# Kernel tuning notes

Measured on AMD Instinct MI355X. Metric: run time of the kernel, lower is better.

Reference implementation:

```python
import jax, jax.numpy as jnp
import numpy as np

IN_SIZE = 784
Z_DIM = 128
K_DIM = 8192
BATCH = 16384
ENC_HIDDEN = [512, 256]          # EncoderMLP default
DEC_SIZES = [Z_DIM, 256, 512, 784]  # DecoderMLP default: [latent, *hidden]


def _linear(x, w, b):
    return x @ w + b


def find_nearest(query, target):
    # Faithful to: sqrt(sum((Q-T)^2, -1)).min(1)[1]; sqrt is monotone so
    # argmin of squared distance is identical. Computed via the GEMM
    # expansion instead of materializing the (N,K,D) broadcast tensor.
    q2 = jnp.sum(query * query, axis=1, keepdims=True)        # [N,1]
    t2 = jnp.sum(target * target, axis=1)                     # [K]
    d2 = q2 - 2.0 * (query @ target.T) + t2[None, :]          # [N,K]
    idx = jnp.argmin(d2, axis=1)
    return target[idx]


def setup_inputs() -> dict:
    key = jax.random.key(0)
    ks = jax.random.split(key, 16)
    s = 0.02
    inp = {"X": jax.random.uniform(ks[0], (BATCH, 1, 28, 28), dtype=jnp.float32)}
    # Encoder: 784 -> 512 -> 256 (mlp blocks, ReLU) -> 128 (plain Linear)
    enc_sizes = [IN_SIZE] + ENC_HIDDEN + [Z_DIM]
    for i, (din, dout) in enumerate(zip(enc_sizes, enc_sizes[1:]), 1):
        inp[f"enc_w{i}"] = s * jax.random.normal(ks[i], (din, dout), dtype=jnp.float32)
        inp[f"enc_b{i}"] = jnp.zeros((dout,), dtype=jnp.float32)
    # Codebook
    inp["codebook"] = jax.random.normal(ks[8], (K_DIM, Z_DIM), dtype=jnp.float32)
    # Decoder: 128 -> 256 -> 512 -> 784 (mlp blocks, ReLU) + sigmoid out
    for i, (din, dout) in enumerate(zip(DEC_SIZES, DEC_SIZES[1:]), 1):
        inp[f"dec_w{i}"] = s * jax.random.normal(ks[8 + i], (din, dout), dtype=jnp.float32)
        inp[f"dec_b{i}"] = jnp.zeros((dout,), dtype=jnp.float32)
    return inp


def reference(X, enc_w1, enc_b1, enc_w2, enc_b2, enc_w3, enc_b3, codebook,
              dec_w1, dec_b1, dec_w2, dec_b2, dec_w3, dec_b3):
    x = X.reshape(-1, IN_SIZE)
    # Encoder (mlp_block = Linear+ReLU, final layer plain Linear)
    h = jax.nn.relu(_linear(x, enc_w1, enc_b1))
    h = jax.nn.relu(_linear(h, enc_w2, enc_b2))
    z_enc = _linear(h, enc_w3, enc_b3)                         # [N, Z]
    # Nearest codebook vector for each encoding
    z_dec = find_nearest(z_enc, codebook)                      # [N, Z]
    # Decoder
    d = jax.nn.relu(_linear(z_dec, dec_w1, dec_b1))
    d = jax.nn.relu(_linear(d, dec_w2, dec_b2))
    d = jax.nn.relu(_linear(d, dec_w3, dec_b3))
    x_recon = jax.nn.sigmoid(d).reshape(-1, 1, 28, 28)
    # Nearest encoding for each codebook vector (for embedding loss)
    z_enc_for_embd = find_nearest(codebook, z_enc)             # [K, Z]
    return (x_recon, z_enc, z_dec, z_enc_for_embd)
```

## Files before the change

kernel.cpp:

```cpp
#include <hip/hip_runtime.h>
#include <math.h>

using u16 = unsigned short;
using u32 = unsigned int;
using u64 = unsigned long long;

typedef __bf16 bf16x8 __attribute__((ext_vector_type(8)));
typedef short  s16x8  __attribute__((ext_vector_type(8)));
typedef float  f32x4  __attribute__((ext_vector_type(4)));

__device__ __forceinline__ float b2f(u16 u){
  union { u32 i; float f; } x; x.i = ((u32)u) << 16; return x.f;
}
__device__ __forceinline__ u16 f2b(float f){
  union { float f; u32 i; } x; x.f = f;
  u32 i = x.i;
  u32 r = (i + 0x7fffu + ((i >> 16) & 1u)) >> 16;
  return (u16)r;
}
__device__ __forceinline__ f32x4 mfma16(s16x8 a, s16x8 b, f32x4 c){
  return __builtin_amdgcn_mfma_f32_16x16x32_bf16(
      __builtin_bit_cast(bf16x8, a), __builtin_bit_cast(bf16x8, b), c, 0, 0, 0);
}
__device__ __forceinline__ u64 shfl_xor_u64(u64 v, int m){
  int lo = __shfl_xor((int)(u32)v, m);
  int hi = __shfl_xor((int)(u32)(v >> 32), m);
  return ((u64)(u32)hi << 32) | (u32)lo;
}
__device__ __forceinline__ u64 umin64(u64 a, u64 b){ return a < b ? a : b; }
__device__ __forceinline__ u64 packmin(float v, int idx){
  u32 b = __float_as_uint(v);
  b = (b & 0x80000000u) ? ~b : (b | 0x80000000u);
  return ((u64)b << 32) | (u32)idx;
}

__global__ __launch_bounds__(256) void canary_k(float* out, float code){
  out[threadIdx.x] = code;
}

__global__ __launch_bounds__(256) void prep_weights(
    const float* __restrict__ w1, const float* __restrict__ w2, const float* __restrict__ w3,
    const float* __restrict__ dw1, const float* __restrict__ dw2, const float* __restrict__ dw3,
    const float* __restrict__ cb,
    u16* __restrict__ o1h, u16* __restrict__ o1l, u16* __restrict__ o2h, u16* __restrict__ o2l,
    u16* __restrict__ o3h, u16* __restrict__ o3l, u16* __restrict__ o4h, u16* __restrict__ o4l,
    u16* __restrict__ o5h, u16* __restrict__ o5l, u16* __restrict__ o6h, u16* __restrict__ o6l,
    u16* __restrict__ cbh, u16* __restrict__ cbl)
{
  size_t o = (size_t)blockIdx.x * 256 + threadIdx.x;
  if (o >= 1155072){
    size_t e = o - 1155072;
    if (e >= 1048576) return;
    float v = cb[e];
    u16 h = f2b(v);
    cbh[e] = h;
    cbl[e] = f2b(v - b2f(h));
    return;
  }
  const float* src; u16 *hi, *lo; int K, N, Kp; size_t base;
  if      (o <  425984){ src=w1;  hi=o1h; lo=o1l; K=784; N=512; Kp=832; base=0; }
  else if (o <  557056){ src=w2;  hi=o2h; lo=o2l; K=512; N=256; Kp=512; base=425984; }
  else if (o <  589824){ src=w3;  hi=o3h; lo=o3l; K=256; N=128; Kp=256; base=557056; }
  else if (o <  622592){ src=dw1; hi=o4h; lo=o4l; K=128; N=256; Kp=128; base=589824; }
  else if (o <  753664){ src=dw2; hi=o5h; lo=o5l; K=256; N=512; Kp=256; base=622592; }
  else                 { src=dw3; hi=o6h; lo=o6l; K=512; N=784; Kp=512; base=753664; }
  size_t e = o - base;
  int n = (int)(e / Kp), kp = (int)(e % Kp);
  u16 h = 0, l = 0;
  if (kp < K){
    float v = src[(size_t)kp * N + n];
    h = f2b(v);
    l = f2b(v - b2f(h));
  }
  hi[e] = h; lo[e] = l;
}

__global__ __launch_bounds__(256) void norms_all(const float* __restrict__ z, const float* __restrict__ cb,
                                                 float* __restrict__ q2, float* __restrict__ t2){
  int i = blockIdx.x * 256 + threadIdx.x;
  const float* src; float* dst;
  if (i < 16384){ src = z + (size_t)i * 128; dst = q2 + i; }
  else { int j = i - 16384; src = cb + (size_t)j * 128; dst = t2 + j; }
  const float4* r = (const float4*)src;
  float s = 0.f;
  for (int k = 0; k < 32; k++){
    float4 p = r[k];
    s += p.x * p.x + p.y * p.y + p.z * p.z + p.w * p.w;
  }
  *dst = s;
}

template<int ACT, int OUTP>
__global__ __launch_bounds__(256, 2) void gemm_af32(
    const float* __restrict__ A, const u16* __restrict__ B0, const u16* __restrict__ B1,
    const float* __restrict__ bias, float* __restrict__ Cf,
    u16* __restrict__ P0, u16* __restrict__ P1,
    int Astr, int KLIM, int Kp, int KT, int N, int nRowsB)
{
  __shared__ __align__(16) u16 Ah[128][72];
  __shared__ __align__(16) u16 Al[128][72];
  __shared__ __align__(16) u16 Bh[128][72];
  __shared__ __align__(16) u16 Bl[128][72];
  const int tid = threadIdx.x;
  const int m0 = blockIdx.y * 128, n0 = blockIdx.x * 128;
  const int wave = tid >> 6, lane = tid & 63;
  const int wm = (wave >> 1) * 64, wn = (wave & 1) * 64;
  const int quad = lane >> 4, l15 = lane & 15;
  f32x4 acc[4][4] = {};

  for (int kt = 0; kt < KT; ++kt){
    const int kb = kt * 64;
    #pragma unroll
    for (int c = 0; c < 8; c++){
      int idx = c * 256 + tid;
      int r = idx >> 4, c4 = (idx & 15) * 4;
      float4 v = make_float4(0.f, 0.f, 0.f, 0.f);
      if (kb + c4 < KLIM)
        v = *(const float4*)(A + (size_t)(m0 + r) * Astr + kb + c4);
      ushort4 h, l;
      h.x = f2b(v.x); l.x = f2b(v.x - b2f(h.x));
      h.y = f2b(v.y); l.y = f2b(v.y - b2f(h.y));
      h.z = f2b(v.z); l.z = f2b(v.z - b2f(h.z));
      h.w = f2b(v.w); l.w = f2b(v.w - b2f(h.w));
      *(ushort4*)&Ah[r][c4] = h;
      *(ushort4*)&Al[r][c4] = l;
    }
    #pragma unroll
    for (int c = 0; c < 4; c++){
      int idx = c * 256 + tid;
      int r = idx >> 3, col = (idx & 7) * 8;
      int rb = n0 + r; rb = rb < nRowsB ? rb : nRowsB - 1;
      *(uint4*)&Bh[r][col] = *(const uint4*)(B0 + (size_t)rb * Kp + kb + col);
      *(uint4*)&Bl[r][col] = *(const uint4*)(B1 + (size_t)rb * Kp + kb + col);
    }
    __syncthreads();
    #pragma unroll
    for (int kh = 0; kh < 2; ++kh){
      s16x8 ah[4], al[4], bh[4], bl[4];
      #pragma unroll
      for (int t4 = 0; t4 < 4; t4++){
        ah[t4] = *(const s16x8*)&Ah[wm + t4 * 16 + l15][kh * 32 + quad * 8];
        al[t4] = *(const s16x8*)&Al[wm + t4 * 16 + l15][kh * 32 + quad * 8];
        bh[t4] = *(const s16x8*)&Bh[wn + t4 * 16 + l15][kh * 32 + quad * 8];
        bl[t4] = *(const s16x8*)&Bl[wn + t4 * 16 + l15][kh * 32 + quad * 8];
      }
      #pragma unroll
      for (int mt = 0; mt < 4; mt++)
        #pragma unroll
        for (int nt = 0; nt < 4; nt++){
          acc[mt][nt] = mfma16(ah[mt], bh[nt], acc[mt][nt]);
          acc[mt][nt] = mfma16(ah[mt], bl[nt], acc[mt][nt]);
          acc[mt][nt] = mfma16(al[mt], bh[nt], acc[mt][nt]);
        }
    }
    __syncthreads();
  }

  float bvs[4]; int cols[4];
  #pragma unroll
  for (int nt = 0; nt < 4; nt++){
    int cN = n0 + wn + nt * 16 + l15;
    cols[nt] = cN;
    int cc = cN < N ? cN : N - 1;
    bvs[nt] = bias[cc];
  }
  #pragma unroll
  for (int mt = 0; mt < 4; mt++){
    int rbase = m0 + wm + mt * 16 + quad * 4;
    #pragma unroll
    for (int nt = 0; nt < 4; nt++){
      if (cols[nt] < N){
        #pragma unroll
        for (int r = 0; r < 4; r++){
          float v = acc[mt][nt][r] + bvs[nt];
          if (ACT >= 1) v = v > 0.f ? v : 0.f;
          if (ACT == 2) v = 1.f / (1.f + expf(-v));
          size_t off = (size_t)(rbase + r) * N + cols[nt];
          if (OUTP == 2){
            P0[off] = f2b(v);
          } else {
            Cf[off] = v;
            if (OUTP == 1){
              u16 h = f2b(v);
              P0[off] = h;
              P1[off] = f2b(v - b2f(h));
            }
          }
        }
      }
    }
  }
}

__global__ __launch_bounds__(256, 1) void dist3(
    const u16* __restrict__ Zh, const u16* __restrict__ Zl,
    const u16* __restrict__ Bh, const u16* __restrict__ Bl,
    const float* __restrict__ q2, const float* __restrict__ t2,
    u64* __restrict__ rowp, u64* __restrict__ colp)
{
  __shared__ u64 sRow[2][128];
  const int tid = threadIdx.x;
  const int i0 = blockIdx.y * 128;
  const int strip = blockIdx.x;
  const int wave = tid >> 6, lane = tid & 63;
  const int wm = (wave >> 1) * 64, wn = (wave & 1) * 64;
  const int quad = lane >> 4, l15 = lane & 15;

  s16x8 zh[2][2][4], zl[2][2][4];
  #pragma unroll
  for (int kb = 0; kb < 2; kb++)
    #pragma unroll
    for (int kh = 0; kh < 2; kh++)
      #pragma unroll
      for (int mt = 0; mt < 4; mt++){
        size_t off = (size_t)(i0 + wm + mt * 16 + l15) * 128 + kb * 64 + kh * 32 + quad * 8;
        zh[kb][kh][mt] = *(const s16x8*)(Zh + off);
        zl[kb][kh][mt] = *(const s16x8*)(Zl + off);
      }
  float qv[4][4];
  #pragma unroll
  for (int mt = 0; mt < 4; mt++)
    #pragma unroll
    for (int r = 0; r < 4; r++)
      qv[mt][r] = q2[i0 + wm + mt * 16 + quad * 4 + r];

  u64 rowm[4][4];
  #pragma unroll
  for (int mt = 0; mt < 4; mt++)
    #pragma unroll
    for (int r = 0; r < 4; r++) rowm[mt][r] = ~0ULL;

  for (int jt = 0; jt < 16; ++jt){
    const int j0 = strip * 2048 + jt * 128;
    f32x4 acc[4][4] = {};
    #pragma unroll
    for (int kb = 0; kb < 2; kb++)
      #pragma unroll
      for (int kh = 0; kh < 2; kh++){
        s16x8 bh[4], bl[4];
        #pragma unroll
        for (int nt = 0; nt < 4; nt++){
          size_t off = (size_t)(j0 + wn + nt * 16 + l15) * 128 + kb * 64 + kh * 32 + quad * 8;
          bh[nt] = *(const s16x8*)(Bh + off);
          bl[nt] = *(const s16x8*)(Bl + off);
        }
        #pragma unroll
        for (int mt = 0; mt < 4; mt++)
          #pragma unroll
          for (int nt = 0; nt < 4; nt++){
            acc[mt][nt] = mfma16(zh[kb][kh][mt], bh[nt], acc[mt][nt]);
            acc[mt][nt] = mfma16(zh[kb][kh][mt], bl[nt], acc[mt][nt]);
            acc[mt][nt] = mfma16(zl[kb][kh][mt], bh[nt], acc[mt][nt]);
            acc[mt][nt] = mfma16(zl[kb][kh][mt], bl[nt], acc[mt][nt]);
          }
      }
    float t2v[4]; int gj[4];
    #pragma unroll
    for (int nt = 0; nt < 4; nt++){
      gj[nt] = j0 + wn + nt * 16 + l15;
      t2v[nt] = t2[gj[nt]];
    }
    #pragma unroll
    for (int mt = 0; mt < 4; mt++){
      #pragma unroll
      for (int r = 0; r < 4; r++){
        float qq = qv[mt][r];
        float rbest = (qq - 2.f * acc[mt][0][r]) + t2v[0];
        int   ridx  = gj[0];
        #pragma unroll
        for (int nt = 1; nt < 4; nt++){
          float v = (qq - 2.f * acc[mt][nt][r]) + t2v[nt];
          if (v < rbest){ rbest = v; ridx = gj[nt]; }
        }
        rowm[mt][r] = umin64(rowm[mt][r], packmin(rbest, ridx));
      }
    }
    #pragma unroll
    for (int nt = 0; nt < 4; nt++){
      float cbest = 3.4e38f; int cidx = 0;
      #pragma unroll
      for (int mt = 0; mt < 4; mt++){
        #pragma unroll
        for (int r = 0; r < 4; r++){
          float vc = (t2v[nt] - 2.f * acc[mt][nt][r]) + qv[mt][r];
          if (vc < cbest){ cbest = vc; cidx = i0 + wm + mt * 16 + quad * 4 + r; }
        }
      }
      u64 p = packmin(cbest, cidx);
      p = umin64(p, shfl_xor_u64(p, 16));
      p = umin64(p, shfl_xor_u64(p, 32));
      if (quad == 0)
        colp[(size_t)(blockIdx.y * 2 + (wave >> 1)) * 8192 + gj[nt]] = p;
    }
  }

  #pragma unroll
  for (int mt = 0; mt < 4; mt++)
    #pragma unroll
    for (int r = 0; r < 4; r++){
      u64 p = rowm[mt][r];
      p = umin64(p, shfl_xor_u64(p, 1));
      p = umin64(p, shfl_xor_u64(p, 2));
      p = umin64(p, shfl_xor_u64(p, 4));
      p = umin64(p, shfl_xor_u64(p, 8));
      rowm[mt][r] = p;
    }
  if (l15 == 0){
    #pragma unroll
    for (int mt = 0; mt < 4; mt++)
      #pragma unroll
      for (int r = 0; r < 4; r++)
        sRow[wave & 1][wm + mt * 16 + quad * 4 + r] = rowm[mt][r];
  }
  __syncthreads();
  if (tid < 128)
    rowp[(size_t)strip * 16384 + i0 + tid] = umin64(sRow[0][tid], sRow[1][tid]);
}

__global__ __launch_bounds__(256) void reduce_rc(
    const u64* __restrict__ rowp, const u64* __restrict__ colp,
    const float* __restrict__ cb, const float* __restrict__ zenc,
    float* __restrict__ zdec, float* __restrict__ zembd, int* __restrict__ rowidx)
{
  int tid = threadIdx.x;
  __shared__ u64 s[4][64];
  __shared__ int sidx[64];
  if (blockIdx.x < 256){
    int base = blockIdx.x * 64;
    int n = base + (tid & 63);
    u64 best = ~0ULL;
    for (int p = tid >> 6; p < 4; p += 4)
      best = umin64(best, rowp[(size_t)p * 16384 + n]);
    s[tid >> 6][tid & 63] = best;
    __syncthreads();
    if (tid < 64){
      u64 b = umin64(umin64(s[0][tid], s[1][tid]), umin64(s[2][tid], s[3][tid]));
      int idx = (int)(b & 0xffffffffULL);
      idx = idx < 0 ? 0 : (idx > 8191 ? 8191 : idx);
      sidx[tid] = idx;
      rowidx[base + tid] = idx;
    }
    __syncthreads();
    for (int q = 0; q < 32; q++){
      int e = q * 256 + tid; int r = e >> 7, c = e & 127;
      zdec[(size_t)(base + r) * 128 + c] = cb[(size_t)sidx[r] * 128 + c];
    }
  } else {
    int base = (blockIdx.x - 256) * 64;
    int n = base + (tid & 63);
    u64 best = ~0ULL;
    for (int p = tid >> 6; p < 256; p += 4)
      best = umin64(best, colp[(size_t)p * 8192 + n]);
    s[tid >> 6][tid & 63] = best;
    __syncthreads();
    if (tid < 64){
      u64 b = umin64(umin64(s[0][tid], s[1][tid]), umin64(s[2][tid], s[3][tid]));
      int idx = (int)(b & 0xffffffffULL);
      idx = idx < 0 ? 0 : (idx > 16383 ? 16383 : idx);
      sidx[tid] = idx;
    }
    __syncthreads();
    for (int q = 0; q < 32; q++){
      int e = q * 256 + tid; int r = e >> 7, c = e & 127;
      zembd[(size_t)(base + r) * 128 + c] = zenc[(size_t)sidx[r] * 128 + c];
    }
  }
}

__global__ __launch_bounds__(256) void gather_xrec(
    const u16* __restrict__ xdecb, const int* __restrict__ rowidx, float* __restrict__ xrec)
{
  size_t o = (size_t)blockIdx.x * 256 + threadIdx.x;
  int row = (int)(o / 784), c = (int)(o % 784);
  int idx = rowidx[row];
  idx = idx < 0 ? 0 : (idx > 8191 ? 8191 : idx);
  xrec[o] = b2f(xdecb[(size_t)idx * 784 + c]);
}

extern "C" void kernel_launch(void* const* d_in, const int* in_sizes, int n_in,
                              void* d_out, int out_size, void* d_ws, size_t ws_size,
                              hipStream_t stream){
  const float* X   = (const float*)d_in[0];
  const float* w1  = (const float*)d_in[1];  const float* b1  = (const float*)d_in[2];
  const float* w2  = (const float*)d_in[3];  const float* b2  = (const float*)d_in[4];
  const float* w3  = (const float*)d_in[5];  const float* b3  = (const float*)d_in[6];
  const float* cb  = (const float*)d_in[7];
  const float* dw1 = (const float*)d_in[8];  const float* db1 = (const float*)d_in[9];
  const float* dw2 = (const float*)d_in[10]; const float* db2 = (const float*)d_in[11];
  const float* dw3 = (const float*)d_in[12]; const float* db3 = (const float*)d_in[13];

  float* out   = (float*)d_out;
  float* xrec  = out;
  float* zenc  = out + 12845056;
  float* zdec  = zenc + 2097152;
  float* zembd = zdec + 2097152;

  const size_t NEEDED = 22085632;
  if (ws_size < NEEDED){
    canary_k<<<1, 256, 0, stream>>>(out, 1000.0f + (float)(ws_size >> 20));
    return;
  }

  char* ob = (char*)d_out;
  float* h1   = (float*)(ob + 0);
  float* g2   = (float*)(ob + 0);
  u16*   zhi  = (u16*)(ob + 33554432);
  u16*   zlo  = (u16*)(ob + 37748736);
  u16*   cbhi = (u16*)(ob + 41943040);
  u16*   cblo = (u16*)(ob + 44040192);

  char* w = (char*)d_ws;
  u16* W1Th = (u16*)(w + 0);        u16* W1Tl = (u16*)(w + 851968);
  u16* W2Th = (u16*)(w + 1703936);  u16* W2Tl = (u16*)(w + 1966080);
  u16* W3Th = (u16*)(w + 2228224);  u16* W3Tl = (u16*)(w + 2293760);
  u16* D1Th = (u16*)(w + 2359296);  u16* D1Tl = (u16*)(w + 2424832);
  u16* D2Th = (u16*)(w + 2490368);  u16* D2Tl = (u16*)(w + 2752512);
  u16* D3Th = (u16*)(w + 3014656);  u16* D3Tl = (u16*)(w + 3817472);
  float* q2f = (float*)(w + 4620288);
  float* t2f = (float*)(w + 4685824);
  int*  rowi = (int*)(w + 4718592);
  u64*  rowp = (u64*)(w + 4784128);
  float* h2   = (float*)(w + 5308416);
  u64*  colp  = (u64*)(w + 5308416);
  float* g1   = (float*)(w + 13697024);
  u16*  xdecb = (u16*)(w + 5308416);

  prep_weights<<<8608, 256, 0, stream>>>(w1, w2, w3, dw1, dw2, dw3, cb,
      W1Th, W1Tl, W2Th, W2Tl, W3Th, W3Tl, D1Th, D1Tl, D2Th, D2Tl, D3Th, D3Tl, cbhi, cblo);

  gemm_af32<1, 0><<<dim3(4, 128), 256, 0, stream>>>(X,  W1Th, W1Tl, b1, h1,   nullptr, nullptr, 784, 784, 832, 13, 512, 512);
  gemm_af32<1, 0><<<dim3(2, 128), 256, 0, stream>>>(h1, W2Th, W2Tl, b2, h2,   nullptr, nullptr, 512, 512, 512,  8, 256, 256);
  gemm_af32<0, 1><<<dim3(1, 128), 256, 0, stream>>>(h2, W3Th, W3Tl, b3, zenc, zhi,     zlo,     256, 256, 256,  4, 128, 128);

  norms_all<<<96, 256, 0, stream>>>(zenc, cb, q2f, t2f);

  dist3<<<dim3(4, 128), 256, 0, stream>>>(zhi, zlo, cbhi, cblo, q2f, t2f, rowp, colp);

  reduce_rc<<<384, 256, 0, stream>>>(rowp, colp, cb, zenc, zdec, zembd, rowi);

  gemm_af32<1, 0><<<dim3(2, 64), 256, 0, stream>>>(cb, D1Th, D1Tl, db1, g1, nullptr, nullptr, 128, 128, 128, 2, 256, 256);
  gemm_af32<1, 0><<<dim3(4, 64), 256, 0, stream>>>(g1, D2Th, D2Tl, db2, g2, nullptr, nullptr, 256, 256, 256, 4, 512, 512);
  gemm_af32<2, 2><<<dim3(7, 64), 256, 0, stream>>>(g2, D3Th, D3Tl, db3, nullptr, xdecb, nullptr, 512, 512, 512, 8, 784, 784);

  gather_xrec<<<50176, 256, 0, stream>>>(xdecb, rowi, xrec);
}
```

Measured before the change: 595.6 us.

## Software-pipeline codebook fragment loads and defer epilogue in dist3 kernel

Restructures the dist3 tile loop so that B-fragment loads for the next k-slice (and the next tile's first slice) are issued while the current slice's MFMAs run, using a double-buffered register fragment set. The row/column argmin epilogue for the previous tile is moved ahead of the current tile's MFMAs, which lets memory latency and epilogue ALU work overlap with matrix instructions. The cost is higher register pressure from the double buffer plus a live accumulator across iterations, and an extra epilogue after the loop for the last tile.

New measurement: 601.7 us. Within noise of the previous version (+1.0%).

```diff
diff --git a/kernel.cpp b/kernel.cpp
--- a/kernel.cpp
+++ b/kernel.cpp
@@ -192,6 +192,39 @@
   }
 }
 
+struct BFrags { s16x8 h[4], l[4]; };
+
+__device__ __forceinline__ void load_slice(
+    const u16* __restrict__ Bh, const u16* __restrict__ Bl,
+    int j0, int wn, int l15, int quad, int kb, int kh, BFrags& f)
+{
+  #pragma unroll
+  for (int nt = 0; nt < 4; nt++){
+    size_t off = (size_t)(j0 + wn + nt * 16 + l15) * 128 + kb * 64 + kh * 32 + quad * 8;
+    f.h[nt] = *(const s16x8*)(Bh + off);
+    f.l[nt] = *(const s16x8*)(Bl + off);
+  }
+}
+
+template<bool FIRST>
+__device__ __forceinline__ void mfma_slice(
+    const s16x8 zh[4], const s16x8 zl[4], const BFrags& f, f32x4 acc[4][4])
+{
+  #pragma unroll
+  for (int mt = 0; mt < 4; mt++)
+    #pragma unroll
+    for (int nt = 0; nt < 4; nt++){
+      f32x4 c;
+      if (FIRST){ c.x = 0.f; c.y = 0.f; c.z = 0.f; c.w = 0.f; }
+      else c = acc[mt][nt];
+      c = mfma16(zh[mt], f.h[nt], c);
+      c = mfma16(zh[mt], f.l[nt], c);
+      c = mfma16(zl[mt], f.h[nt], c);
+      c = mfma16(zl[mt], f.l[nt], c);
+      acc[mt][nt] = c;
+    }
+}
+
 __global__ __launch_bounds__(256, 1) void dist3(
     const u16* __restrict__ Zh, const u16* __restrict__ Zl,
     const u16* __restrict__ Bh, const u16* __restrict__ Bl,
@@ -206,7 +239,7 @@
   const int wm = (wave >> 1) * 64, wn = (wave & 1) * 64;
   const int quad = lane >> 4, l15 = lane & 15;
 
-  s16x8 zh[2][2][4], zl[2][2][4];
+  s16x8 zh[4][4], zl[4][4];
   #pragma unroll
   for (int kb = 0; kb < 2; kb++)
     #pragma unroll
@@ -214,8 +247,8 @@
       #pragma unroll
       for (int mt = 0; mt < 4; mt++){
         size_t off = (size_t)(i0 + wm + mt * 16 + l15) * 128 + kb * 64 + kh * 32 + quad * 8;
-        zh[kb][kh][mt] = *(const s16x8*)(Zh + off);
-        zl[kb][kh][mt] = *(const s16x8*)(Zl + off);
+        zh[kb * 2 + kh][mt] = *(const s16x8*)(Zh + off);
+        zl[kb * 2 + kh][mt] = *(const s16x8*)(Zl + off);
       }
   float qv[4][4];
   #pragma unroll
@@ -230,34 +263,74 @@
     #pragma unroll
     for (int r = 0; r < 4; r++) rowm[mt][r] = ~0ULL;
 
+  f32x4 acc[4][4];
+  BFrags fb[2];
+  const int jbase = strip * 2048;
+  load_slice(Bh, Bl, jbase, wn, l15, quad, 0, 0, fb[0]);
+
   for (int jt = 0; jt < 16; ++jt){
-    const int j0 = strip * 2048 + jt * 128;
-    f32x4 acc[4][4] = {};
-    #pragma unroll
-    for (int kb = 0; kb < 2; kb++)
-      #pragma unroll
-      for (int kh = 0; kh < 2; kh++){
-        s16x8 bh[4], bl[4];
+    const int j0 = jbase + jt * 128;
+    const int j0n = jbase + ((jt + 1) & 15) * 128;
+
+    load_slice(Bh, Bl, j0, wn, l15, quad, 0, 1, fb[1]);
+
+    if (jt > 0){
+      const int j0p = j0 - 128;
+      float t2v[4]; int gj[4];
+      #pragma unroll
+      for (int nt = 0; nt < 4; nt++){
+        gj[nt] = j0p + wn + nt * 16 + l15;
+        t2v[nt] = t2[gj[nt]];
+      }
+      #pragma unroll
+      for (int mt = 0; mt < 4; mt++){
         #pragma unroll
-        for (int nt = 0; nt < 4; nt++){
-          size_t off = (size_t)(j0 + wn + nt * 16 + l15) * 128 + kb * 64 + kh * 32 + quad * 8;
-          bh[nt] = *(const s16x8*)(Bh + off);
-          bl[nt] = *(const s16x8*)(Bl + off);
+        for (int r = 0; r < 4; r++){
+          float qq = qv[mt][r];
+          float rbest = (qq - 2.f * acc[mt][0][r]) + t2v[0];
+          int   ridx  = gj[0];
+          #pragma unroll
+          for (int nt = 1; nt < 4; nt++){
+            float v = (qq - 2.f * acc[mt][nt][r]) + t2v[nt];
+            if (v < rbest){ rbest = v; ridx = gj[nt]; }
+          }
+          rowm[mt][r] = umin64(rowm[mt][r], packmin(rbest, ridx));
         }
+      }
+      #pragma unroll
+      for (int nt = 0; nt < 4; nt++){
+        float cbest = 3.4e38f; int cidx = 0;
         #pragma unroll
-        for (int mt = 0; mt < 4; mt++)
+        for (int mt = 0; mt < 4; mt++){
           #pragma unroll
-          for (int nt = 0; nt < 4; nt++){
-            acc[mt][nt] = mfma16(zh[kb][kh][mt], bh[nt], acc[mt][nt]);
-            acc[mt][nt] = mfma16(zh[kb][kh][mt], bl[nt], acc[mt][nt]);
-            acc[mt][nt] = mfma16(zl[kb][kh][mt], bh[nt], acc[mt][nt]);
-            acc[mt][nt] = mfma16(zl[kb][kh][mt], bl[nt], acc[mt][nt]);
+          for (int r = 0; r < 4; r++){
+            float vc = (t2v[nt] - 2.f * acc[mt][nt][r]) + qv[mt][r];
+            if (vc < cbest){ cbest = vc; cidx = i0 + wm + mt * 16 + quad * 4 + r; }
           }
-      }
+        }
+        u64 p = packmin(cbest, cidx);
+        p = umin64(p, shfl_xor_u64(p, 16));
+        p = umin64(p, shfl_xor_u64(p, 32));
+        if (quad == 0)
+          colp[(size_t)(blockIdx.y * 2 + (wave >> 1)) * 8192 + gj[nt]] = p;
+      }
+    }
+
+    mfma_slice<true >(zh[0], zl[0], fb[0], acc);
+    load_slice(Bh, Bl, j0, wn, l15, quad, 1, 0, fb[0]);
+    mfma_slice<false>(zh[1], zl[1], fb[1], acc);
+    load_slice(Bh, Bl, j0, wn, l15, quad, 1, 1, fb[1]);
+    mfma_slice<false>(zh[2], zl[2], fb[0], acc);
+    load_slice(Bh, Bl, j0n, wn, l15, quad, 0, 0, fb[0]);
+    mfma_slice<false>(zh[3], zl[3], fb[1], acc);
+  }
+
+  {
+    const int j0p = jbase + 15 * 128;
     float t2v[4]; int gj[4];
     #pragma unroll
     for (int nt = 0; nt < 4; nt++){
-      gj[nt] = j0 + wn + nt * 16 + l15;
+      gj[nt] = j0p + wn + nt * 16 + l15;
       t2v[nt] = t2[gj[nt]];
     }
     #pragma unroll
```
